# Kernel optimization log

Measured on AMD Instinct MI355X. Metric: run time of the kernel, lower is better.

## Reference

```python
import jax, jax.numpy as jnp
import numpy as np
import math

N_HEAD = 12
BLOCK = 256  # local attention block size (ls)
EPS = 1e-6


def _rotate(x):
    # pairs (a, b) -> (-b, a) over last dim (matches rotate_embeddings)
    a = x[..., 0::2]
    b = x[..., 1::2]
    return jnp.stack([-b, a], axis=-1).reshape(x.shape)


def setup_inputs() -> dict:
    key = jax.random.key(0)
    k1, k2, k3 = jax.random.split(key, 3)
    B, T, C = 4, 8192, 768
    s = 0.02
    return {
        "x": jax.random.normal(k1, (B, T, C), jnp.float32),
        "w_qkv": jax.random.normal(k2, (C, 3 * C), jnp.float32) * s,
        "w_ln": jnp.ones((C,), jnp.float32),
        "w_proj": jax.random.normal(k3, (C, C), jnp.float32) * s,
    }


def reference(x, w_qkv, w_ln, w_proj):
    B, T, C = x.shape
    nh, ls = N_HEAD, BLOCK
    hd = C // nh
    ng = T // ls

    xb = x.reshape(B, ng, ls, C)
    qkv = xb @ w_qkv                                   # (B,ng,ls,3C)
    q, k, v = jnp.split(qkv, 3, axis=-1)

    # QK RMSNorm over full embedding dim (before head split)
    def rms(t):
        return t * jax.lax.rsqrt(jnp.mean(t * t, axis=-1, keepdims=True) + EPS) * w_ln
    q, k = rms(q), rms(k)

    # split heads: (B,ng,nh,ls,hd)
    def heads(t):
        return jnp.swapaxes(t.reshape(B, ng, ls, nh, hd), 2, 3)
    q, k, v = heads(q), heads(k), heads(v)

    # RoPE (repo layout: freqs tiled via cat((ts,ts)), interleaved pair rotation)
    pos = 10000.0 ** ((-2.0 * jnp.arange(0, hd, 2, dtype=jnp.float32) - 1.0) / hd)
    ts = jnp.arange(ls, dtype=jnp.float32)[:, None] * pos[None, :]   # (ls, hd/2)
    rot = jnp.concatenate([ts, ts], axis=-1)                          # (ls, hd)
    cos, sin = jnp.cos(rot), jnp.sin(rot)
    q = q * cos + _rotate(q) * sin
    k = k * cos + _rotate(k) * sin

    # block-causal scores: causal only within each local block
    scale = 1.0 / math.sqrt(hd)
    att = jnp.einsum('bgnqd,bgnkd->bgnqk', q, k) * scale              # (B,ng,nh,ls,ls)
    mask = jnp.tril(jnp.ones((ls, ls), dtype=bool))
    att = jnp.where(mask, att, -jnp.finfo(att.dtype).max)
    att = jax.nn.softmax(att, axis=-1)
    y = jnp.einsum('bgnqk,bgnkd->bgnqd', att, v)                      # (B,ng,nh,ls,hd)

    y = jnp.swapaxes(y, 2, 3).reshape(B, ng, ls, C)
    y = y @ w_proj
    return y.reshape(B, T, C)
```

## Files before the change

kernel.cpp:

```cpp
#include <hip/hip_runtime.h>
#include <math.h>

typedef __attribute__((ext_vector_type(8))) short bf16x8;
typedef __attribute__((ext_vector_type(4))) short bf16x4;
typedef __attribute__((ext_vector_type(2))) short bf16x2;
typedef __attribute__((ext_vector_type(4))) float f32x4;
typedef __attribute__((ext_vector_type(16))) float f32x16;

#define NH 12
#define HD 64
#define C0 768
#define C3 2304
#define LS 256
#define KT12 12

static __device__ __forceinline__ float bf2f(short u) {
  union { unsigned int i; float f; } c;
  c.i = ((unsigned int)(unsigned short)u) << 16;
  return c.f;
}
static __device__ __forceinline__ short f2bf(float f) {
  union { float f; unsigned int i; } c; c.f = f;
  unsigned int x = c.i;
  x += 0x7fffu + ((x >> 16) & 1u);
  return (short)(x >> 16);
}
static __device__ __forceinline__ unsigned pk2(float a, float b) {
  return (unsigned)(unsigned short)f2bf(a) | ((unsigned)(unsigned short)f2bf(b) << 16);
}

static __device__ __forceinline__ void gload_lds16(const short* g, const short* l) {
  unsigned long long ga = (unsigned long long)g;
  unsigned int la = (unsigned int)(unsigned long long)l;
  __builtin_amdgcn_global_load_lds(
      (const __attribute__((address_space(1))) void*)ga,
      (__attribute__((address_space(3))) void*)la, 16, 0, 0);
}

__global__ __launch_bounds__(256) void cast_pack_A_kernel(const float* __restrict__ x,
                                                          short* __restrict__ Apk) {
  __shared__ short sb[256 * 64];
  int bm = blockIdx.x, kt = blockIdx.y, t = threadIdx.x;
#pragma unroll
  for (int i = 0; i < 8; ++i) {
    int seg = i * 256 + t;
    int row = seg >> 3, sc = (seg & 7) * 8;
    const float* src = x + ((long)(bm * 256 + row)) * C0 + kt * 64 + sc;
    float4 v0 = *(const float4*)src;
    float4 v1 = *(const float4*)(src + 4);
    short* d = &sb[row * 64 + sc];
    d[0] = f2bf(v0.x); d[1] = f2bf(v0.y); d[2] = f2bf(v0.z); d[3] = f2bf(v0.w);
    d[4] = f2bf(v1.x); d[5] = f2bf(v1.y); d[6] = f2bf(v1.z); d[7] = f2bf(v1.w);
  }
  __syncthreads();
#pragma unroll
  for (int i = 0; i < 8; ++i) {
    int c = i * 256 + t;
    int l = c & 63, f = c >> 6;
    int ks = f & 3, mt = (f >> 2) & 3, mh = f >> 4;
    int row = mh * 128 + mt * 32 + (l & 31);
    int kk = ks * 16 + (l >> 5) * 8;
    bf16x8 v = *(bf16x8*)&sb[row * 64 + kk];
    *(bf16x8*)&Apk[(((long)bm * KT12 + kt) * 2048 + c) * 8] = v;
  }
}

__global__ __launch_bounds__(256) void cast_pack_B_kernel(const float* __restrict__ w,
                                                          short* __restrict__ Bpk, int N) {
  __shared__ short sb[256 * 64];
  int bn = blockIdx.x, kt = blockIdx.y, t = threadIdx.x;
#pragma unroll
  for (int i = 0; i < 8; ++i) {
    int seg = i * 256 + t;
    int k = seg >> 5, nc = (seg & 31) * 8;
    const float* src = w + ((long)(kt * 64 + k)) * N + bn * 256 + nc;
    float4 v0 = *(const float4*)src;
    float4 v1 = *(const float4*)(src + 4);
    sb[(nc + 0) * 64 + k] = f2bf(v0.x); sb[(nc + 1) * 64 + k] = f2bf(v0.y);
    sb[(nc + 2) * 64 + k] = f2bf(v0.z); sb[(nc + 3) * 64 + k] = f2bf(v0.w);
    sb[(nc + 4) * 64 + k] = f2bf(v1.x); sb[(nc + 5) * 64 + k] = f2bf(v1.y);
    sb[(nc + 6) * 64 + k] = f2bf(v1.z); sb[(nc + 7) * 64 + k] = f2bf(v1.w);
  }
  __syncthreads();
#pragma unroll
  for (int i = 0; i < 8; ++i) {
    int c = i * 256 + t;
    int l = c & 63, f = c >> 6;
    int ks = f & 3, nt = (f >> 2) & 1, wng = f >> 3;
    int col = wng * 64 + nt * 32 + (l & 31);
    int kk = ks * 16 + (l >> 5) * 8;
    bf16x8 v = *(bf16x8*)&sb[col * 64 + kk];
    *(bf16x8*)&Bpk[(((long)bn * KT12 + kt) * 2048 + c) * 8] = v;
  }
}

__global__ void rope_tab_kernel(float* __restrict__ cost, float* __restrict__ sint) {
  int t = blockIdx.x, d = threadIdx.x;
  int i = d & 31;
  float freq = powf(10000.0f, -(float)(4 * i + 1) / 64.0f);
  float th = (float)t * freq;
  cost[t * 64 + d] = cosf(th);
  sint[t * 64 + d] = sinf(th);
}

#define PH_OPEN                                        \
  __builtin_amdgcn_s_barrier();                        \
  asm volatile("s_waitcnt lgkmcnt(0)" ::: "memory");   \
  __builtin_amdgcn_sched_barrier(0);                   \
  __builtin_amdgcn_s_setprio(1);
#define PH_MID __builtin_amdgcn_s_setprio(0);
#define PH_CLOSE                                       \
  asm volatile("s_waitcnt vmcnt(2)" ::: "memory");     \
  __builtin_amdgcn_s_barrier();
#define MM8(ASET, BSET, MP, NT)                                                     \
  { _Pragma("unroll") for (int m2_ = 0; m2_ < 2; ++m2_)                             \
      _Pragma("unroll") for (int ks_ = 0; ks_ < 4; ++ks_)                           \
        acc[(MP)*2 + m2_][NT] = __builtin_amdgcn_mfma_f32_32x32x16_bf16(            \
            ASET[m2_ * 4 + ks_], BSET[ks_], acc[(MP)*2 + m2_][NT], 0, 0, 0); }

template <int OUT_F32, int PACKED_A>
__global__ __launch_bounds__(512, 2) void gemm32_kernel(const short* __restrict__ Apk,
                                                        const short* __restrict__ Bpk,
                                                        const short* __restrict__ Arm,
                                                        void* __restrict__ Cout,
                                                        int N, int K, int nbn) {
  __shared__ short lds[65536];
  int t = threadIdx.x, lane = t & 63, wave = t >> 6;
  int wm = (wave >> 2) * 128, wng = wave & 3, wn = wng * 64, mh = wave >> 2;
  int id = blockIdx.x;
  int cpx = gridDim.x >> 3;
  int sw = (id & 7) * cpx + (id >> 3);
  int bm = sw / nbn, bn = sw % nbn;

  f32x16 acc[4][2];
#pragma unroll
  for (int m = 0; m < 4; ++m)
#pragma unroll
    for (int n = 0; n < 2; ++n)
#pragma unroll
      for (int r = 0; r < 16; ++r) acc[m][n][r] = 0.f;

  bf16x8 a0[8], a1[8], b0[4], b1[4];

  auto STAGE = [&](int s) {
    if (s >= 4 * KT12) return;
    int q = s & 3, Ts = s >> 2;
    int bb = (Ts & 1) * 32768;
    if (q < 2) {
      if (PACKED_A) {
        int c = q * 1024 + t;
        const short* src = Apk + ((long)bm * KT12 + Ts) * 16384 + (long)c * 8;
        gload_lds16(src, &lds[bb + c * 8]);
        gload_lds16(src + 4096, &lds[bb + (c + 512) * 8]);
      } else {
        int row = q * 128 + (t >> 3);
        int cr = q * 1024 + t;
        const short* s1 = Arm + ((long)(bm * 256 + row)) * K + Ts * 64 + ((t & 7) ^ (row & 7)) * 8;
        gload_lds16(s1, &lds[bb + cr * 8]);
        int row2 = row + 64;
        const short* s2 = Arm + ((long)(bm * 256 + row2)) * K + Ts * 64 + ((t & 7) ^ (row2 & 7)) * 8;
        gload_lds16(s2, &lds[bb + (cr + 512) * 8]);
      }
    } else {
      int c = (q - 2) * 1024 + t;
      const short* src = Bpk + ((long)bn * KT12 + Ts) * 16384 + (long)c * 8;
      gload_lds16(src, &lds[bb + 16384 + c * 8]);
      gload_lds16(src + 4096, &lds[bb + 16384 + (c + 512) * 8]);
    }
  };
  auto LDA = [&](bf16x8* d, int b, int mhalf) {
    if (PACKED_A) {
#pragma unroll
      for (int m2 = 0; m2 < 2; ++m2)
#pragma unroll
        for (int ks = 0; ks < 4; ++ks)
          d[m2 * 4 + ks] =
              *(bf16x8*)&lds[b * 32768 + ((mh * 16 + (mhalf * 2 + m2) * 4 + ks) * 64 + lane) * 8];
    } else {
#pragma unroll
      for (int m2 = 0; m2 < 2; ++m2)
#pragma unroll
        for (int ks = 0; ks < 4; ++ks) {
          int row = wm + (mhalf * 2 + m2) * 32 + (lane & 31);
          int g = (ks * 2 + (lane >> 5)) ^ (row & 7);
          d[m2 * 4 + ks] = *(bf16x8*)&lds[b * 32768 + row * 64 + g * 8];
        }
    }
  };
  auto LDB = [&](bf16x8* d, int b, int nt) {
#pragma unroll
    for (int ks = 0; ks < 4; ++ks)
      d[ks] = *(bf16x8*)&lds[b * 32768 + 16384 + ((wng * 8 + nt * 4 + ks) * 64 + lane) * 8];
  };

  for (int s = 0; s < 7; ++s) STAGE(s);
  asm volatile("s_waitcnt vmcnt(6)" ::: "memory");
  __builtin_amdgcn_s_barrier();
  LDA(a0, 0, 0);
  LDB(b0, 0, 0);
  LDB(b1, 0, 1);

  for (int it = 0; it < KT12 / 2; ++it) {
    int P0 = 8 * it;
    PH_OPEN; MM8(a0, b0, 0, 0); PH_MID;
    LDA(a1, 0, 1); STAGE(P0 + 7); PH_CLOSE;
    PH_OPEN; MM8(a0, b1, 0, 1); PH_MID;
    LDA(a0, 1, 0); STAGE(P0 + 8); PH_CLOSE;
    PH_OPEN; MM8(a1, b0, 1, 0); PH_MID;
    LDB(b0, 1, 0); STAGE(P0 + 9); PH_CLOSE;
    PH_OPEN; MM8(a1, b1, 1, 1); PH_MID;
    LDB(b1, 1, 1); STAGE(P0 + 10); PH_CLOSE;
    PH_OPEN; MM8(a0, b0, 0, 0); PH_MID;
    LDA(a1, 1, 1); STAGE(P0 + 11); PH_CLOSE;
    PH_OPEN; MM8(a0, b1, 0, 1); PH_MID;
    LDA(a0, 0, 0); STAGE(P0 + 12); PH_CLOSE;
    PH_OPEN; MM8(a1, b0, 1, 0); PH_MID;
    LDB(b0, 0, 0); STAGE(P0 + 13); PH_CLOSE;
    PH_OPEN; MM8(a1, b1, 1, 1); PH_MID;
    LDB(b1, 0, 1); STAGE(P0 + 14); PH_CLOSE;
  }

  long crow0 = (long)bm * 256 + wm;
  long ccol0 = (long)bn * 256 + wn;
  int rbase = 4 * (lane >> 5);
  int cl = lane & 31;
#pragma unroll
  for (int mt = 0; mt < 4; ++mt)
#pragma unroll
    for (int nt = 0; nt < 2; ++nt)
#pragma unroll
      for (int reg = 0; reg < 16; ++reg) {
        long row = crow0 + mt * 32 + (reg & 3) + 8 * (reg >> 2) + rbase;
        long col = ccol0 + nt * 32 + cl;
        float v = acc[mt][nt][reg];
        if (OUT_F32) ((float*)Cout)[row * N + col] = v;
        else ((short*)Cout)[row * N + col] = f2bf(v);
      }
}

__global__ __launch_bounds__(384) void norm_rope_kernel(short* __restrict__ QKV,
    const float* __restrict__ w_ln, const float* __restrict__ cost,
    const float* __restrict__ sint) {
  int row = blockIdx.x;
  int t = row & 255;
  int i = threadIdx.x;
  bool isq = i < 192;
  int e0 = (i - (isq ? 0 : 192)) * 4;
  long off = (long)row * C3 + (isq ? 0 : C0) + e0;
  bf16x4 v4 = *(const bf16x4*)&QKV[off];
  float a = bf2f(v4.x), b = bf2f(v4.y), c = bf2f(v4.z), d = bf2f(v4.w);
  float ss = a * a + b * b + c * c + d * d;
#pragma unroll
  for (int o = 32; o > 0; o >>= 1) ss += __shfl_down(ss, o);
  __shared__ float red[6];
  if ((i & 63) == 0) red[i >> 6] = ss;
  __syncthreads();
  float s3 = isq ? (red[0] + red[1] + red[2]) : (red[3] + red[4] + red[5]);
  float r = rsqrtf(s3 * (1.0f / 768.0f) + 1e-6f);
  float4 wl = *(const float4*)&w_ln[e0];
  int d0 = e0 & 63;
  float4 cs = *(const float4*)&cost[t * 64 + d0];
  float4 sn = *(const float4*)&sint[t * 64 + d0];
  float n0 = a * r * wl.x, n1 = b * r * wl.y, n2 = c * r * wl.z, n3 = d * r * wl.w;
  bf16x4 o;
  o.x = f2bf(n0 * cs.x - n1 * sn.x);
  o.y = f2bf(n1 * cs.y + n0 * sn.y);
  o.z = f2bf(n2 * cs.z - n3 * sn.z);
  o.w = f2bf(n3 * cs.w + n2 * sn.w);
  *(bf16x4*)&QKV[off] = o;
}

__global__ __launch_bounds__(512, 3) void attn_kernel(const short* __restrict__ QKV,
                                                      short* __restrict__ Y) {
  __shared__ short Ks[256 * 64];
  __shared__ short Vt[64 * 256];
  int blk = blockIdx.x;
  int bg = blk / NH, h = blk % NH;
  const long base = (long)bg * LS * C3 + h * HD;
  int tid = threadIdx.x, lane = tid & 63, wave = tid >> 6;
  int lr = lane & 15, lg = lane >> 4;

#pragma unroll
  for (int it = 0; it < 4; ++it) {
    int q = it * 512 + tid;
    int row = q >> 3, cp = q & 7;
    int gcp = cp ^ (row & 7);
    gload_lds16(QKV + base + (long)row * C3 + C0 + gcp * 8, &Ks[q * 8]);
  }
#pragma unroll
  for (int it = 0; it < 8; ++it) {
    int e = tid * 4 + it * 2048;
    int k = e >> 6, n = e & 63;
    bf16x4 v = *(const bf16x4*)&QKV[base + (long)k * C3 + 2 * C0 + n];
#pragma unroll
    for (int j = 0; j < 4; ++j) {
      int nn = n + j;
      Vt[nn * 256 + (((k >> 3) ^ (nn & 7)) << 3) + (k & 7)] = v[j];
    }
  }
  asm volatile("s_waitcnt vmcnt(0)" ::: "memory");
  __syncthreads();

  int addrA = (((lane >> 4) & 1) * 32 + lr) * 4;
  int addrB = addrA + 64;
  bool selhi = (lane & 32) != 0;

  for (int tt = 0; tt < 2; ++tt) {
    int tile = (tt == 0) ? wave : (15 - wave);
    int m0 = tile * 16;
    bf16x8 qf[2];
#pragma unroll
    for (int ks = 0; ks < 2; ++ks)
      qf[ks] = *(const bf16x8*)&QKV[base + (long)(m0 + lr) * C3 + ks * 32 + lg * 8];

    f32x4 zero4 = {0.f, 0.f, 0.f, 0.f};
    f32x4 accs[16];
#pragma unroll
    for (int n = 0; n < 16; ++n) accs[n] = zero4;

    __builtin_amdgcn_s_setprio(1);
#pragma unroll
    for (int n = 0; n < 16; ++n) {
      if (n <= tile) {
        int row = n * 16 + lr, sw = row & 7;
        bf16x8 k0 = *(bf16x8*)&Ks[row * 64 + ((lg ^ sw) << 3)];
        bf16x8 k1 = *(bf16x8*)&Ks[row * 64 + (((4 + lg) ^ sw) << 3)];
        accs[n] = __builtin_amdgcn_mfma_f32_16x16x32_bf16(k0, qf[0], accs[n], 0, 0, 0);
        accs[n] = __builtin_amdgcn_mfma_f32_16x16x32_bf16(k1, qf[1], accs[n], 0, 0, 0);
      }
    }
    __builtin_amdgcn_s_setprio(0);

    float tm[16];
#pragma unroll
    for (int n = 0; n < 16; ++n) {
      if (n <= tile) {
        if (n == tile) {
#pragma unroll
          for (int r = 0; r < 4; ++r)
            accs[n][r] = (lg * 4 + r <= lr) ? accs[n][r] : -1e30f;
        }
        float m01 = fmaxf(accs[n][0], accs[n][1]);
        float m23 = fmaxf(accs[n][2], accs[n][3]);
        tm[n] = fmaxf(m01, m23);
      } else {
        tm[n] = -1e30f;
      }
    }
#pragma unroll
    for (int st = 1; st < 16; st <<= 1)
#pragma unroll
      for (int j = 0; j < 16; j += 2 * st) tm[j] = fmaxf(tm[j], tm[j + st]);
    float mloc = tm[0];
    mloc = fmaxf(mloc, __shfl_xor(mloc, 16));
    mloc = fmaxf(mloc, __shfl_xor(mloc, 32));

    float ts[16];
#pragma unroll
    for (int n = 0; n < 16; ++n) {
      if (n <= tile) {
#pragma unroll
        for (int r = 0; r < 4; ++r) accs[n][r] = __expf((accs[n][r] - mloc) * 0.125f);
        float s01 = accs[n][0] + accs[n][1];
        float s23 = accs[n][2] + accs[n][3];
        ts[n] = s01 + s23;
      } else {
        ts[n] = 0.f;
      }
    }
#pragma unroll
    for (int st = 1; st < 16; st <<= 1)
#pragma unroll
      for (int j = 0; j < 16; j += 2 * st) ts[j] += ts[j + st];
    float s = ts[0];
    s += __shfl_xor(s, 16);
    s += __shfl_xor(s, 32);
    float rs = 1.0f / s;
    float rv[4];
#pragma unroll
    for (int r = 0; r < 4; ++r) {
      union { float f; int i; } c; c.f = rs;
      union { int i; float f; } o;
      o.i = __builtin_amdgcn_ds_bpermute((lg * 4 + r) * 4, c.i);
      rv[r] = o.f;
    }

    int ktmax = (m0 + 15) >> 5;
    f32x4 yacc[4];
#pragma unroll
    for (int n2 = 0; n2 < 4; ++n2) yacc[n2] = zero4;
#pragma unroll
    for (int kt = 0; kt < 8; ++kt) {
      if (kt <= ktmax) {
        int n0 = 2 * kt, n1 = 2 * kt + 1;
        unsigned a01_0 = pk2(accs[n0][0], accs[n0][1]);
        unsigned a23_0 = pk2(accs[n0][2], accs[n0][3]);
        unsigned a01_1 = (n1 <= tile) ? pk2(accs[n1][0], accs[n1][1]) : 0u;
        unsigned a23_1 = (n1 <= tile) ? pk2(accs[n1][2], accs[n1][3]) : 0u;
        union { unsigned u[4]; bf16x8 v; } af;
        unsigned g0a = (unsigned)__builtin_amdgcn_ds_bpermute(addrA, (int)a01_0);
        unsigned g0b = (unsigned)__builtin_amdgcn_ds_bpermute(addrA, (int)a01_1);
        unsigned g1a = (unsigned)__builtin_amdgcn_ds_bpermute(addrA, (int)a23_0);
        unsigned g1b = (unsigned)__builtin_amdgcn_ds_bpermute(addrA, (int)a23_1);
        unsigned g2a = (unsigned)__builtin_amdgcn_ds_bpermute(addrB, (int)a01_0);
        unsigned g2b = (unsigned)__builtin_amdgcn_ds_bpermute(addrB, (int)a01_1);
        unsigned g3a = (unsigned)__builtin_amdgcn_ds_bpermute(addrB, (int)a23_0);
        unsigned g3b = (unsigned)__builtin_amdgcn_ds_bpermute(addrB, (int)a23_1);
        af.u[0] = selhi ? g0b : g0a;
        af.u[1] = selhi ? g1b : g1a;
        af.u[2] = selhi ? g2b : g2a;
        af.u[3] = selhi ? g3b : g3a;
        int ac = kt * 32 + lg * 8;
        __builtin_amdgcn_s_setprio(1);
#pragma unroll
        for (int n2 = 0; n2 < 4; ++n2) {
          int vn = n2 * 16 + lr;
          bf16x8 vb = *(bf16x8*)&Vt[vn * 256 + (((ac >> 3) ^ (vn & 7)) << 3)];
          yacc[n2] = __builtin_amdgcn_mfma_f32_16x16x32_bf16(af.v, vb, yacc[n2], 0, 0, 0);
        }
        __builtin_amdgcn_s_setprio(0);
      }
    }

#pragma unroll
    for (int n2 = 0; n2 < 4; ++n2) {
#pragma unroll
      for (int r = 0; r < 4; ++r) {
        int row = m0 + lg * 4 + r, d = n2 * 16 + lr;
        Y[((long)(bg * LS + row)) * C0 + h * HD + d] = f2bf(yacc[n2][r] * rv[r]);
      }
    }
  }
}

extern "C" void kernel_launch(void* const* d_in, const int* in_sizes, int n_in,
                              void* d_out, int out_size, void* d_ws, size_t ws_size,
                              hipStream_t stream) {
  (void)in_sizes; (void)n_in; (void)out_size; (void)ws_size;
  const float* x = (const float*)d_in[0];
  const float* w_qkv = (const float*)d_in[1];
  const float* w_ln = (const float*)d_in[2];
  const float* w_proj = (const float*)d_in[3];
  float* out = (float*)d_out;

  char* ws = (char*)d_ws;
  short* Apk     = (short*)(ws + 0);
  short* QKV     = (short*)(ws + 50331648);
  short* Yb      = (short*)(ws + 201326592);
  short* WqkvPk  = (short*)(ws + 251658240);
  short* WprojPk = (short*)(ws + 255197184);
  float* cost    = (float*)(ws + 256376832);
  float* sint    = (float*)(ws + 256442368);

  cast_pack_A_kernel<<<dim3(128, KT12), 256, 0, stream>>>(x, Apk);
  cast_pack_B_kernel<<<dim3(9, KT12), 256, 0, stream>>>(w_qkv, WqkvPk, C3);
  cast_pack_B_kernel<<<dim3(3, KT12), 256, 0, stream>>>(w_proj, WprojPk, C0);
  rope_tab_kernel<<<256, 64, 0, stream>>>(cost, sint);

  gemm32_kernel<0, 1><<<128 * 9, 512, 0, stream>>>(Apk, WqkvPk, nullptr, QKV,
                                                   C3, C0, 9);
  norm_rope_kernel<<<32768, 384, 0, stream>>>(QKV, w_ln, cost, sint);
  attn_kernel<<<128 * NH, 512, 0, stream>>>(QKV, Yb);
  gemm32_kernel<1, 0><<<128 * 3, 512, 0, stream>>>(nullptr, WprojPk, Yb, out,
                                                   C0, C0, 3);
}
```

Measured before the change: 373.0 us.

## Replace A packing with plain cast and add 128-tile output projection GEMM

Replaces the packed A-layout cast kernel with a simple elementwise fp32-to-bf16 cast, so the QKV GEMM now reads row-major activations through its existing row-major A path. Adds a new 128x128-tile GEMM kernel with double-buffered, XOR-swizzled LDS staging for the output projection, launched on 1536 blocks instead of 384 so the GPU is better filled. The weight pack kernel is templated to produce the narrower 128-column B tiles this GEMM needs. The row-major A path may cost more LDS traffic in the QKV GEMM than the pre-packed layout did.

```diff
diff --git a/kernel.cpp b/kernel.cpp
--- a/kernel.cpp
+++ b/kernel.cpp
@@ -37,43 +37,28 @@
       (__attribute__((address_space(3))) void*)la, 16, 0, 0);
 }
 
-__global__ __launch_bounds__(256) void cast_pack_A_kernel(const float* __restrict__ x,
-                                                          short* __restrict__ Apk) {
-  __shared__ short sb[256 * 64];
-  int bm = blockIdx.x, kt = blockIdx.y, t = threadIdx.x;
-#pragma unroll
-  for (int i = 0; i < 8; ++i) {
-    int seg = i * 256 + t;
-    int row = seg >> 3, sc = (seg & 7) * 8;
-    const float* src = x + ((long)(bm * 256 + row)) * C0 + kt * 64 + sc;
-    float4 v0 = *(const float4*)src;
-    float4 v1 = *(const float4*)(src + 4);
-    short* d = &sb[row * 64 + sc];
-    d[0] = f2bf(v0.x); d[1] = f2bf(v0.y); d[2] = f2bf(v0.z); d[3] = f2bf(v0.w);
-    d[4] = f2bf(v1.x); d[5] = f2bf(v1.y); d[6] = f2bf(v1.z); d[7] = f2bf(v1.w);
-  }
-  __syncthreads();
-#pragma unroll
-  for (int i = 0; i < 8; ++i) {
-    int c = i * 256 + t;
-    int l = c & 63, f = c >> 6;
-    int ks = f & 3, mt = (f >> 2) & 3, mh = f >> 4;
-    int row = mh * 128 + mt * 32 + (l & 31);
-    int kk = ks * 16 + (l >> 5) * 8;
-    bf16x8 v = *(bf16x8*)&sb[row * 64 + kk];
-    *(bf16x8*)&Apk[(((long)bm * KT12 + kt) * 2048 + c) * 8] = v;
-  }
-}
-
+__global__ __launch_bounds__(256) void cast_kernel(const float* __restrict__ in,
+                                                   short* __restrict__ out, int nquads) {
+  int i = blockIdx.x * blockDim.x + threadIdx.x;
+  int stride = gridDim.x * blockDim.x;
+  for (; i < nquads; i += stride) {
+    float4 v = ((const float4*)in)[i];
+    bf16x4 o = { f2bf(v.x), f2bf(v.y), f2bf(v.z), f2bf(v.w) };
+    ((bf16x4*)out)[i] = o;
+  }
+}
+
+template <int WNG>
 __global__ __launch_bounds__(256) void cast_pack_B_kernel(const float* __restrict__ w,
                                                           short* __restrict__ Bpk, int N) {
-  __shared__ short sb[256 * 64];
+  __shared__ short sb[WNG * 64 * 64];
   int bn = blockIdx.x, kt = blockIdx.y, t = threadIdx.x;
 #pragma unroll
-  for (int i = 0; i < 8; ++i) {
+  for (int i = 0; i < WNG * 2; ++i) {
     int seg = i * 256 + t;
-    int k = seg >> 5, nc = (seg & 31) * 8;
-    const float* src = w + ((long)(kt * 64 + k)) * N + bn * 256 + nc;
+    int k = seg / (WNG * 8);
+    int nc = (seg % (WNG * 8)) * 8;
+    const float* src = w + ((long)(kt * 64 + k)) * N + bn * (WNG * 64) + nc;
     float4 v0 = *(const float4*)src;
     float4 v1 = *(const float4*)(src + 4);
     sb[(nc + 0) * 64 + k] = f2bf(v0.x); sb[(nc + 1) * 64 + k] = f2bf(v0.y);
@@ -83,14 +68,14 @@
   }
   __syncthreads();
 #pragma unroll
-  for (int i = 0; i < 8; ++i) {
+  for (int i = 0; i < WNG * 2; ++i) {
     int c = i * 256 + t;
     int l = c & 63, f = c >> 6;
     int ks = f & 3, nt = (f >> 2) & 1, wng = f >> 3;
     int col = wng * 64 + nt * 32 + (l & 31);
     int kk = ks * 16 + (l >> 5) * 8;
     bf16x8 v = *(bf16x8*)&sb[col * 64 + kk];
-    *(bf16x8*)&Bpk[(((long)bn * KT12 + kt) * 2048 + c) * 8] = v;
+    *(bf16x8*)&Bpk[(((long)bn * KT12 + kt) * (WNG * 512) + c) * 8] = v;
   }
 }
 
@@ -232,6 +217,96 @@
       for (int reg = 0; reg < 16; ++reg) {
         long row = crow0 + mt * 32 + (reg & 3) + 8 * (reg >> 2) + rbase;
         long col = ccol0 + nt * 32 + cl;
+        float v = acc[mt][nt][reg];
+        if (OUT_F32) ((float*)Cout)[row * N + col] = v;
+        else ((short*)Cout)[row * N + col] = f2bf(v);
+      }
+}
+
+template <int OUT_F32>
+__global__ __launch_bounds__(256, 2) void gemm128_kernel(const short* __restrict__ Arm,
+                                                         const short* __restrict__ Bpk,
+                                                         void* __restrict__ Cout,
+                                                         int N, int K, int nbn) {
+  __shared__ short lds[32768];
+  int t = threadIdx.x, lane = t & 63, wave = t >> 6;
+  int wm = (wave >> 1) * 64, wng = wave & 1;
+  int id = blockIdx.x;
+  int cpx = gridDim.x >> 3;
+  int sw = (id & 7) * cpx + (id >> 3);
+  int bm = sw / nbn, bn = sw % nbn;
+  int l31 = lane & 31, lh = lane >> 5;
+
+  f32x16 acc[2][2];
+#pragma unroll
+  for (int m = 0; m < 2; ++m)
+#pragma unroll
+    for (int n = 0; n < 2; ++n)
+#pragma unroll
+      for (int r = 0; r < 16; ++r) acc[m][n][r] = 0.f;
+
+  auto STAGE = [&](int T) {
+    int bb = (T & 1) * 16384;
+#pragma unroll
+    for (int i = 0; i < 4; ++i) {
+      int q = i * 256 + t;
+      int row = q >> 3, cp = q & 7;
+      const short* ga = Arm + ((long)(bm * 128 + row)) * K + T * 64 + ((cp ^ (row & 7)) * 8);
+      gload_lds16(ga, &lds[bb + q * 8]);
+      const short* gb = Bpk + ((long)bn * KT12 + T) * 8192 + (long)q * 8;
+      gload_lds16(gb, &lds[bb + 8192 + q * 8]);
+    }
+  };
+
+  STAGE(0);
+  asm volatile("s_waitcnt vmcnt(0)" ::: "memory");
+  __builtin_amdgcn_s_barrier();
+
+  for (int T = 0; T < KT12; ++T) {
+    int bb = (T & 1) * 16384;
+    if (T + 1 < KT12) STAGE(T + 1);
+    bf16x8 a[2][4], b[2][4];
+#pragma unroll
+    for (int mt = 0; mt < 2; ++mt) {
+      int row = wm + mt * 32 + l31;
+      int s8 = row & 7;
+#pragma unroll
+      for (int ks = 0; ks < 4; ++ks) {
+        int g = (ks * 2 + lh) ^ s8;
+        a[mt][ks] = *(bf16x8*)&lds[bb + row * 64 + g * 8];
+      }
+    }
+#pragma unroll
+    for (int nt = 0; nt < 2; ++nt)
+#pragma unroll
+      for (int ks = 0; ks < 4; ++ks)
+        b[nt][ks] = *(bf16x8*)&lds[bb + 8192 + (((wng * 2 + nt) * 4 + ks) * 64 + lane) * 8];
+    __builtin_amdgcn_s_setprio(1);
+#pragma unroll
+    for (int mt = 0; mt < 2; ++mt)
+#pragma unroll
+      for (int nt = 0; nt < 2; ++nt)
+#pragma unroll
+        for (int ks = 0; ks < 4; ++ks)
+          acc[mt][nt] = __builtin_amdgcn_mfma_f32_32x32x16_bf16(a[mt][ks], b[nt][ks],
+                                                                acc[mt][nt], 0, 0, 0);
+    __builtin_amdgcn_s_setprio(0);
+    asm volatile("s_waitcnt lgkmcnt(0)" ::: "memory");
+    asm volatile("s_waitcnt vmcnt(0)" ::: "memory");
+    __builtin_amdgcn_s_barrier();
+  }
+
+  long crow0 = (long)bm * 128 + wm;
+  long ccol0 = (long)bn * 128 + wng * 64;
+  int rbase = 4 * lh;
+#pragma unroll
+  for (int mt = 0; mt < 2; ++mt)
+#pragma unroll
+    for (int nt = 0; nt < 2; ++nt)
+#pragma unroll
+      for (int reg = 0; reg < 16; ++reg) {
+        long row = crow0 + mt * 32 + (reg & 3) + 8 * (reg >> 2) + rbase;
+        long col = ccol0 + nt * 32 + l31;
         float v = acc[mt][nt][reg];
         if (OUT_F32) ((float*)Cout)[row * N + col] = v;
         else ((short*)Cout)[row * N + col] = f2bf(v);
@@ -444,7 +519,7 @@
   float* out = (float*)d_out;
 
   char* ws = (char*)d_ws;
-  short* Apk     = (short*)(ws + 0);
+  short* Xb      = (short*)(ws + 0);
   short* QKV     = (short*)(ws + 50331648);
   short* Yb      = (short*)(ws + 201326592);
   short* WqkvPk  = (short*)(ws + 251658240);
@@ -452,15 +527,14 @@
   float* cost    = (float*)(ws + 256376832);
   float* sint    = (float*)(ws + 256442368);
 
-  cast_pack_A_kernel<<<dim3(128, KT12), 256, 0, stream>>>(x, Apk);
-  cast_pack_B_kernel<<<dim3(9, KT12), 256, 0, stream>>>(w_qkv, WqkvPk, C3);
-  cast_pack_B_kernel<<<dim3(3, KT12), 256, 0, stream>>>(w_proj, WprojPk, C0);
+  cast_kernel<<<2048, 256, 0, stream>>>(x, Xb, (4 * 8192 * C0) / 4);
+  cast_pack_B_kernel<4><<<dim3(9, KT12), 256, 0, stream>>>(w_qkv, WqkvPk, C3);
+  cast_pack_B_kernel<2><<<dim3(6, KT12), 256, 0, stream>>>(w_proj, WprojPk, C0);
   rope_tab_kernel<<<256, 64, 0, stream>>>(cost, sint);
 
-  gemm32_kernel<0, 1><<<128 * 9, 512, 0, stream>>>(Apk, WqkvPk, nullptr, QKV,
+  gemm32_kernel<0, 0><<<128 * 9, 512, 0, stream>>>(nullptr, WqkvPk, Xb, QKV,
                                                    C3, C0, 9);
   norm_rope_kernel<<<32768, 384, 0, stream>>>(QKV, w_ln, cost, sint);
   attn_kernel<<<128 * NH, 512, 0, stream>>>(QKV, Yb);
-  gemm32_kernel<1, 0><<<128 * 3, 512, 0, stream>>>(nullptr, WprojPk, Yb, out,
-                                                   C0, C0, 3);
-}
+  gemm128_kernel<1><<<256 * 6, 256, 0, stream>>>(Yb, WprojPk, out, C0, C0, 6);
+}
```

Result: no change. 372.0 us (-0.3%).
